# Kernel optimization log

Hardware: AMD Instinct MI355X
Metric: run time of the kernel (lower is better)

Reference implementation:

```python
import jax, jax.numpy as jnp
import numpy as np

ALPHA, GAMMA = 0.25, 2.0
IMG_FM, STRIDE = 96, 8


def _make_anchors():
    sizes = np.array([32.0, 64.0, 128.0], np.float32)
    ratios = np.array([0.5, 1.0, 2.0], np.float32)
    c = (np.arange(IMG_FM, dtype=np.float32) + 0.5) * STRIDE
    cy, cx = np.meshgrid(c, c, indexing="ij")
    hs = (sizes[:, None] * np.sqrt(ratios)[None, :]).reshape(-1)
    ws = (sizes[:, None] / np.sqrt(ratios)[None, :]).reshape(-1)
    y1 = cy[..., None] - hs / 2
    x1 = cx[..., None] - ws / 2
    y2 = cy[..., None] + hs / 2
    x2 = cx[..., None] + ws / 2
    # anchor layout (y1, x1, y2, x2), matching anchor_widths = a[:,3]-a[:,1]
    return np.stack([y1, x1, y2, x2], axis=-1).reshape(-1, 4).astype(np.float32)


def setup_inputs() -> dict:
    B, C, N = 4, 80, 32
    EMB, IDS, H, W = 128, 500, IMG_FM, IMG_FM
    A = IMG_FM * IMG_FM * 9
    key = jax.random.key(0)
    ks = jax.random.split(key, 8)
    cls = jax.random.uniform(ks[0], (B, A, C), jnp.float32)
    reg = jax.random.normal(ks[1], (B, A, 4), jnp.float32)
    emb = jax.random.normal(ks[2], (B, EMB, H, W), jnp.float32)
    # boxes (x1, y1, x2, y2); keep x1+x2 < 768 so (x1+x2)//8 < 96
    xy1 = jax.random.uniform(ks[3], (B, N, 2), jnp.float32, 0.0, 280.0)
    wh = jax.random.uniform(ks[4], (B, N, 2), jnp.float32, 16.0, 96.0)
    boxes = jnp.concatenate([xy1, jnp.minimum(xy1 + wh, 350.0)], axis=-1)
    labels = jax.random.randint(ks[5], (B, N), 0, C).astype(jnp.int64)
    reids = jax.random.randint(ks[6], (B, N), 0, IDS).astype(jnp.int64)
    W_track = jax.random.normal(ks[7], (EMB, IDS), jnp.float32) * 0.05
    b_track = jnp.zeros((IDS,), jnp.float32)
    anchors = jnp.asarray(_make_anchors())[None]  # [1, A, 4]
    return {
        "classifications": cls,
        "regressions": reg,
        "anchors": anchors,
        "embeddings": emb,
        "gt_bboxes_2d": boxes,
        "gt_labels": labels,
        "gt_reids": reids,
        "W_track": W_track,
        "b_track": b_track,
        "emb_scale": jnp.asarray(10.0, jnp.float32),
    }


def reference(classifications, regressions, anchors, embeddings, gt_bboxes_2d,
              gt_labels, gt_reids, W_track, b_track, emb_scale):
    anchor = anchors[0]                                   # [A,4] (y1,x1,y2,x2)
    aw = anchor[:, 3] - anchor[:, 1]
    ah = anchor[:, 2] - anchor[:, 0]
    acx = anchor[:, 1] + 0.5 * aw
    acy = anchor[:, 0] + 0.5 * ah
    num_classes = classifications.shape[-1]

    def per_image(cls_p, reg, emb, boxes, labels, reids):
        cls_p = jnp.clip(cls_p, 1e-4, 1.0 - 1e-4)         # [A,C]
        # ---- IoU: anchor (y1,x1,y2,x2) vs gt (x1,y1,x2,y2), verbatim calc_iou ----
        area_b = (boxes[:, 2] - boxes[:, 0]) * (boxes[:, 3] - boxes[:, 1])  # [N]
        iw = jnp.clip(jnp.minimum(anchor[:, 3:4], boxes[:, 2]) - jnp.maximum(anchor[:, 1:2], boxes[:, 0]), 0.0)
        ih = jnp.clip(jnp.minimum(anchor[:, 2:3], boxes[:, 3]) - jnp.maximum(anchor[:, 0:1], boxes[:, 1]), 0.0)
        inter = iw * ih                                   # [A,N]
        ua = jnp.clip(((anchor[:, 2] - anchor[:, 0]) * (anchor[:, 3] - anchor[:, 1]))[:, None] + area_b - inter, 1e-8)
        iou = inter / ua                                  # [A,N]
        iou_max = iou.max(axis=1)                         # [A]
        iou_arg = iou.argmax(axis=1)                      # [A]
        pos = iou_max >= 0.5
        neg = iou_max < 0.4
        num_pos = pos.sum().astype(cls_p.dtype)
        # ---- focal classification loss ----
        assigned_lab = labels[iou_arg]                    # [A]
        onehot = jax.nn.one_hot(assigned_lab, num_classes, dtype=cls_p.dtype)
        targets = jnp.where(pos[:, None], onehot,
                            jnp.where(neg[:, None], 0.0, -1.0))
        is_one = targets == 1.0
        af = jnp.where(is_one, ALPHA, 1.0 - ALPHA)
        fw = af * jnp.where(is_one, 1.0 - cls_p, cls_p) ** GAMMA
        bce = -(targets * jnp.log(cls_p) + (1.0 - targets) * jnp.log(1.0 - cls_p))
        cls_loss = jnp.where(targets != -1.0, fw * bce, 0.0).sum() / jnp.maximum(num_pos, 1.0)
        ab = boxes[iou_arg]                               # [A,4]
        gw = ab[:, 2] - ab[:, 0]
        gh = ab[:, 3] - ab[:, 1]
        gcx = ab[:, 0] + 0.5 * gw
        gcy = ab[:, 1] + 0.5 * gh
        gw = jnp.clip(gw, 1.0)
        gh = jnp.clip(gh, 1.0)
        tdy = (gcy - acy) / ah
        tdx = (gcx - acx) / aw
        tdh = jnp.log(gh / ah)
        tdw = jnp.log(gw / aw)
        tgt = jnp.stack([tdy, tdx, tdh, tdw], axis=1)     # [A,4]
        d = jnp.abs(tgt - reg)
        rl = jnp.where(d <= 1.0 / 9.0, 0.5 * 9.0 * d * d, d - 0.5 / 9.0)
        reg_loss = (rl * pos[:, None]).sum() / jnp.maximum(num_pos * 4.0, 1.0)
        # ---- ReID tracking loss ----
        c, h, w = emb.shape
        cx_i = jnp.floor((boxes[:, 0] + boxes[:, 2]) / 8.0)  # faithful (x1+x2)//8
        cy_i = jnp.floor((boxes[:, 1] + boxes[:, 3]) / 8.0)
        ind = (cy_i * w + cx_i).astype(jnp.int32)         # [N]
        feat = jnp.transpose(emb, (1, 2, 0)).reshape(h * w, c)[ind]  # [N,c]
        nrm = jnp.sqrt((feat * feat).sum(axis=1, keepdims=True))
        feat = emb_scale * feat / jnp.maximum(nrm, 1e-12)
        logits = feat @ W_track + b_track                 # [N, IDS]
        logp = jax.nn.log_softmax(logits, axis=-1)
        valid = (reids >= 0).astype(logp.dtype)
        ce = -jnp.take_along_axis(logp, jnp.clip(reids, 0).astype(jnp.int32)[:, None], axis=1)[:, 0]
        id_loss = (ce * valid).sum() / jnp.maximum(valid.sum(), 1.0)
        trk_loss = jnp.where(num_pos > 0, id_loss, 0.0)
        return cls_loss, reg_loss, trk_loss

    cls_l, reg_l, trk_l = jax.vmap(per_image)(
        classifications, regressions, embeddings, gt_bboxes_2d, gt_labels, gt_reids)
    return (jnp.mean(cls_l, keepdims=True),
            jnp.mean(reg_l, keepdims=True) * 50.0,
            jnp.mean(trk_l, keepdims=True))
```

## Files before the change

### kernel.cpp

```cpp
#include <hip/hip_runtime.h>
#include <cstdint>
#include <cstddef>

#define A_TOTAL 82944
#define NUM_C   80
#define NBOX    32
#define EMB_C   128
#define IDS     500
#define HW      9216
#define FM_W    96
#define BATCH   4
#define ABLK    256
#define NBLK    (A_TOTAL / ABLK)
#define REID_OFF 8192

typedef float floatx4 __attribute__((ext_vector_type(4)));

__device__ __forceinline__ float wave_sum(float v) {
#pragma unroll
    for (int o = 32; o > 0; o >>= 1) v += __shfl_down(v, o, 64);
    return v;
}
__device__ __forceinline__ float wave_max(float v) {
#pragma unroll
    for (int o = 32; o > 0; o >>= 1) v = fmaxf(v, __shfl_down(v, o, 64));
    return v;
}

__global__ __launch_bounds__(256) void assign_focal_reg_kernel(
    const float* __restrict__ cls, const float* __restrict__ reg,
    const float* __restrict__ anchors, const float* __restrict__ boxes,
    const int* __restrict__ labels, float* __restrict__ part)
{
    const int b   = blockIdx.y;
    const int a0  = blockIdx.x * ABLK;
    const int tid = threadIdx.x;

    __shared__ float4 sbox[NBOX];
    __shared__ int    slab[NBOX];
    __shared__ int    slabenc[ABLK];
    __shared__ float  sgate[ABLK];
    __shared__ float  sred[3][4];

    if (tid < NBOX) {
        sbox[tid] = ((const float4*)boxes)[b * NBOX + tid];
        slab[tid] = labels[b * NBOX + tid];
    }
    __syncthreads();

    const int a = a0 + tid;
    const float4 an = ((const float4*)anchors)[a];
    const float area_a = (an.z - an.x) * (an.w - an.y);
    float best = -1.f; int arg = 0;
#pragma unroll
    for (int n = 0; n < NBOX; ++n) {
        const float4 bx = sbox[n];
        float iw = fmaxf(fminf(an.w, bx.z) - fmaxf(an.y, bx.x), 0.f);
        float ih = fmaxf(fminf(an.z, bx.w) - fmaxf(an.x, bx.y), 0.f);
        float inter = iw * ih;
        float area_b = (bx.z - bx.x) * (bx.w - bx.y);
        float ua  = fmaxf(area_a + area_b - inter, 1e-8f);
        float iou = inter / ua;
        if (iou > best) { best = iou; arg = n; }
    }
    const bool pos = best >= 0.5f;
    const bool neg = best < 0.4f;
    slabenc[tid] = pos ? slab[arg] : -1;
    sgate[tid]   = (pos || neg) ? 1.f : 0.f;

    float reg_part = 0.f, np_part = 0.f;
    if (pos) {
        np_part = 1.f;
        const float4 ab = sbox[arg];
        float gw  = ab.z - ab.x, gh = ab.w - ab.y;
        float gcx = ab.x + 0.5f * gw, gcy = ab.y + 0.5f * gh;
        gw = fmaxf(gw, 1.f); gh = fmaxf(gh, 1.f);
        const float aw  = an.w - an.y, ah = an.z - an.x;
        const float acx = an.y + 0.5f * aw, acy = an.x + 0.5f * ah;
        const float t0 = (gcy - acy) / ah;
        const float t1 = (gcx - acx) / aw;
        const float t2 = logf(gh / ah);
        const float t3 = logf(gw / aw);
        const float4 rg = ((const float4*)reg)[(size_t)b * A_TOTAL + a];
        float dd[4] = { fabsf(t0 - rg.x), fabsf(t1 - rg.y),
                        fabsf(t2 - rg.z), fabsf(t3 - rg.w) };
#pragma unroll
        for (int k = 0; k < 4; ++k) {
            const float d = dd[k];
            reg_part += (d <= (1.f/9.f)) ? (4.5f * d * d) : (d - (0.5f/9.f));
        }
    }
    __syncthreads();

    const floatx4* crow =
        (const floatx4*)(cls + ((size_t)b * A_TOTAL + a0) * NUM_C);
    const float LO = 1e-4f;
    const float HI = (float)(1.0 - 1e-4);
    float cls_part = 0.f;
#pragma unroll
    for (int g = 0; g < 4; ++g) {
        floatx4 buf[5];
#pragma unroll
        for (int i = 0; i < 5; ++i) {
            const int f = tid + (g * 5 + i) * 256;
            buf[i] = __builtin_nontemporal_load(&crow[f]);
        }
#pragma unroll
        for (int i = 0; i < 5; ++i) {
            const int f    = tid + (g * 5 + i) * 256;
            const int row  = f / 20;
            const int col4 = f - row * 20;
            const int rel  = slabenc[row] - col4 * 4;
            const float gate = sgate[row];
            const float pv[4] = { buf[i].x, buf[i].y, buf[i].z, buf[i].w };
            float acc4 = 0.f;
#pragma unroll
            for (int j = 0; j < 4; ++j) {
                const float p  = fminf(fmaxf(pv[j], LO), HI);
                const bool one = (rel == j);
                const float w  = one ? (1.f - p) : p;
                const float af = one ? 0.25f : 0.75f;
                acc4 += af * w * w * (-__logf(1.f - w));
            }
            cls_part = fmaf(acc4, gate, cls_part);
        }
    }

    const float w0 = wave_sum(cls_part);
    const float w1 = wave_sum(reg_part);
    const float w2 = wave_sum(np_part);
    const int wid = tid >> 6, lane = tid & 63;
    if (lane == 0) { sred[0][wid] = w0; sred[1][wid] = w1; sred[2][wid] = w2; }
    __syncthreads();
    if (tid == 0) {
        float* o = part + ((size_t)b * NBLK + blockIdx.x) * 4;
        o[0] = sred[2][0] + sred[2][1] + sred[2][2] + sred[2][3];
        o[1] = sred[0][0] + sred[0][1] + sred[0][2] + sred[0][3];
        o[2] = sred[1][0] + sred[1][1] + sred[1][2] + sred[1][3];
    }
}

__global__ __launch_bounds__(512) void reid_kernel(
    const float* __restrict__ emb, const float* __restrict__ boxes,
    const int* __restrict__ reids, const float* __restrict__ Wt,
    const float* __restrict__ bt, const float* __restrict__ emb_scale,
    float* __restrict__ ws)
{
    const int b   = blockIdx.y;
    const int n   = blockIdx.x;
    const int tid = threadIdx.x;

    __shared__ float sfeat[EMB_C];
    __shared__ float slog[IDS];
    __shared__ float sred[8];
    __shared__ float sb[2];

    const float4 bx = ((const float4*)boxes)[b * NBOX + n];
    const int cx = (int)floorf((bx.x + bx.z) * 0.125f);
    const int cy = (int)floorf((bx.y + bx.w) * 0.125f);
    const int ind = cy * FM_W + cx;

    float sq = 0.f;
    if (tid < EMB_C) {
        const float v = emb[((size_t)b * EMB_C + tid) * HW + ind];
        sfeat[tid] = v;
        sq = v * v;
    }
    const float wsq = wave_sum(sq);
    if ((tid & 63) == 0) sred[tid >> 6] = wsq;
    __syncthreads();
    if (tid == 0) {
        const float nrm = sqrtf(sred[0] + sred[1]);
        sb[0] = emb_scale[0] / fmaxf(nrm, 1e-12f);
    }
    __syncthreads();
    if (tid < EMB_C) sfeat[tid] *= sb[0];
    __syncthreads();

    if (tid < IDS) {
        float al = bt[tid];
#pragma unroll 16
        for (int c = 0; c < EMB_C; ++c) al += sfeat[c] * Wt[c * IDS + tid];
        slog[tid] = al;
    }
    __syncthreads();

    float m = (tid < IDS) ? slog[tid] : -1e30f;
    m = wave_max(m);
    if ((tid & 63) == 0) sred[tid >> 6] = m;
    __syncthreads();
    if (tid == 0) {
        float mm = sred[0];
#pragma unroll
        for (int i = 1; i < 8; ++i) mm = fmaxf(mm, sred[i]);
        sb[1] = mm;
    }
    __syncthreads();
    m = sb[1];

    float se = (tid < IDS) ? expf(slog[tid] - m) : 0.f;
    se = wave_sum(se);
    if ((tid & 63) == 0) sred[tid >> 6] = se;
    __syncthreads();
    if (tid == 0) {
        float sum = 0.f;
#pragma unroll
        for (int i = 0; i < 8; ++i) sum += sred[i];
        const int rid = reids[b * NBOX + n];
        const float valid = (rid >= 0) ? 1.f : 0.f;
        const int t = rid < 0 ? 0 : rid;
        const float ce = -(slog[t] - m - logf(sum));
        float* o = ws + REID_OFF + ((size_t)b * NBOX + n) * 2;
        o[0] = ce * valid;
        o[1] = valid;
    }
}

__global__ __launch_bounds__(256) void finalize_kernel(
    const float* __restrict__ ws, float* __restrict__ out)
{
    __shared__ float s[BATCH][3];
    const int tid  = threadIdx.x;
    const int b    = tid >> 6;
    const int lane = tid & 63;

    float np = 0.f, cl = 0.f, rg = 0.f, ce = 0.f, va = 0.f;
    for (int i = lane; i < NBLK; i += 64) {
        const float* p = ws + ((size_t)b * NBLK + i) * 4;
        np += p[0]; cl += p[1]; rg += p[2];
    }
    if (lane < NBOX) {
        const float* r = ws + REID_OFF + ((size_t)b * NBOX + lane) * 2;
        ce = r[0]; va = r[1];
    }
    np = wave_sum(np); cl = wave_sum(cl); rg = wave_sum(rg);
    ce = wave_sum(ce); va = wave_sum(va);
    if (lane == 0) {
        const float cls_l = cl / fmaxf(np, 1.f);
        const float reg_l = rg / fmaxf(np * 4.f, 1.f);
        const float id_l  = ce / fmaxf(va, 1.f);
        s[b][0] = cls_l;
        s[b][1] = reg_l;
        s[b][2] = (np > 0.f) ? id_l : 0.f;
    }
    __syncthreads();
    if (tid == 0) {
        out[0] = (s[0][0] + s[1][0] + s[2][0] + s[3][0]) * 0.25f;
        out[1] = (s[0][1] + s[1][1] + s[2][1] + s[3][1]) * 0.25f * 50.f;
        out[2] = (s[0][2] + s[1][2] + s[2][2] + s[3][2]) * 0.25f;
    }
}

extern "C" void kernel_launch(void* const* d_in, const int* in_sizes, int n_in,
                              void* d_out, int out_size, void* d_ws, size_t ws_size,
                              hipStream_t stream) {
    const float* cls      = (const float*)d_in[0];
    const float* reg      = (const float*)d_in[1];
    const float* anchors  = (const float*)d_in[2];
    const float* emb      = (const float*)d_in[3];
    const float* boxes    = (const float*)d_in[4];
    const int*   labels   = (const int*)d_in[5];
    const int*   reids    = (const int*)d_in[6];
    const float* Wt       = (const float*)d_in[7];
    const float* bt       = (const float*)d_in[8];
    const float* escale   = (const float*)d_in[9];
    float* out = (float*)d_out;
    float* ws  = (float*)d_ws;

    dim3 g1(NBLK, BATCH);
    assign_focal_reg_kernel<<<g1, dim3(256), 0, stream>>>(cls, reg, anchors,
                                                          boxes, labels, ws);
    dim3 g2(NBOX, BATCH);
    reid_kernel<<<g2, dim3(512), 0, stream>>>(emb, boxes, reids, Wt, bt,
                                              escale, ws);
    finalize_kernel<<<1, 256, 0, stream>>>(ws, out);
}
```

Before: 195.4 us.

## Fuse reid into main kernel, cull IoU via union bbox, simplify focal math

```diff
diff --git a/kernel.cpp b/kernel.cpp
--- a/kernel.cpp
+++ b/kernel.cpp
@@ -27,24 +27,117 @@
     return v;
 }
 
-__global__ __launch_bounds__(256) void assign_focal_reg_kernel(
+__global__ __launch_bounds__(256) void main_kernel(
     const float* __restrict__ cls, const float* __restrict__ reg,
     const float* __restrict__ anchors, const float* __restrict__ boxes,
-    const int* __restrict__ labels, float* __restrict__ part)
+    const int* __restrict__ labels, const float* __restrict__ emb,
+    const int* __restrict__ reids, const float* __restrict__ Wt,
+    const float* __restrict__ bt, const float* __restrict__ emb_scale,
+    float* __restrict__ ws)
 {
     const int b   = blockIdx.y;
-    const int a0  = blockIdx.x * ABLK;
     const int tid = threadIdx.x;
 
     __shared__ float4 sbox[NBOX];
     __shared__ int    slab[NBOX];
+    __shared__ float  sarea[NBOX];
+    __shared__ float4 subb;
     __shared__ int    slabenc[ABLK];
     __shared__ float  sgate[ABLK];
-    __shared__ float  sred[3][4];
-
+    __shared__ float  sred3[3][4];
+    __shared__ float  sfeat[EMB_C];
+    __shared__ float  slog[IDS];
+    __shared__ float  sredR[4];
+    __shared__ float  sb[2];
+
+    if (blockIdx.x >= NBLK) {
+        const int n = blockIdx.x - NBLK;
+        const float4 bx = ((const float4*)boxes)[b * NBOX + n];
+        const int cx = (int)floorf((bx.x + bx.z) * 0.125f);
+        const int cy = (int)floorf((bx.y + bx.w) * 0.125f);
+        const int ind = cy * FM_W + cx;
+
+        float sq = 0.f;
+        if (tid < EMB_C) {
+            const float v = emb[((size_t)b * EMB_C + tid) * HW + ind];
+            sfeat[tid] = v;
+            sq = v * v;
+        }
+        const float wsq = wave_sum(sq);
+        if ((tid & 63) == 0) sredR[tid >> 6] = wsq;
+        __syncthreads();
+        if (tid == 0) {
+            const float nrm = sqrtf(sredR[0] + sredR[1]);
+            sb[0] = emb_scale[0] / fmaxf(nrm, 1e-12f);
+        }
+        __syncthreads();
+        if (tid < EMB_C) sfeat[tid] *= sb[0];
+        __syncthreads();
+
+        const int  j1   = tid + 256;
+        const bool has1 = (j1 < IDS);
+        const float* w0col = Wt + tid;
+        const float* w1col = Wt + (has1 ? j1 : tid);
+        float al0 = bt[tid];
+        float al1 = has1 ? bt[j1] : 0.f;
+#pragma unroll 8
+        for (int c = 0; c < EMB_C; ++c) {
+            const float fv = sfeat[c];
+            al0 = fmaf(fv, w0col[c * IDS], al0);
+            al1 = fmaf(fv, w1col[c * IDS], al1);
+        }
+        slog[tid] = al0;
+        if (has1) slog[j1] = al1;
+
+        float m = has1 ? fmaxf(al0, al1) : al0;
+        m = wave_max(m);
+        if ((tid & 63) == 0) sredR[tid >> 6] = m;
+        __syncthreads();
+        if (tid == 0) {
+            float mm = sredR[0];
+#pragma unroll
+            for (int i = 1; i < 4; ++i) mm = fmaxf(mm, sredR[i]);
+            sb[1] = mm;
+        }
+        __syncthreads();
+        m = sb[1];
+
+        float se = expf(al0 - m) + (has1 ? expf(al1 - m) : 0.f);
+        se = wave_sum(se);
+        if ((tid & 63) == 0) sredR[tid >> 6] = se;
+        __syncthreads();
+        if (tid == 0) {
+            const float sum = sredR[0] + sredR[1] + sredR[2] + sredR[3];
+            const int rid = reids[b * NBOX + n];
+            const float valid = (rid >= 0) ? 1.f : 0.f;
+            const int t = rid < 0 ? 0 : rid;
+            const float ce = -(slog[t] - m - logf(sum));
+            float* o = ws + REID_OFF + ((size_t)b * NBOX + n) * 2;
+            o[0] = ce * valid;
+            o[1] = valid;
+        }
+        return;
+    }
+
+    const int a0 = blockIdx.x * ABLK;
+
+    float ux1 = 1e30f, uy1 = 1e30f, ux2 = -1e30f, uy2 = -1e30f;
     if (tid < NBOX) {
-        sbox[tid] = ((const float4*)boxes)[b * NBOX + tid];
-        slab[tid] = labels[b * NBOX + tid];
+        const float4 bx = ((const float4*)boxes)[b * NBOX + tid];
+        sbox[tid]  = bx;
+        slab[tid]  = labels[b * NBOX + tid];
+        sarea[tid] = (bx.z - bx.x) * (bx.w - bx.y);
+        ux1 = bx.x; uy1 = bx.y; ux2 = bx.z; uy2 = bx.w;
+    }
+    if (tid < 64) {
+#pragma unroll
+        for (int o = 32; o > 0; o >>= 1) {
+            ux1 = fminf(ux1, __shfl_down(ux1, o, 64));
+            uy1 = fminf(uy1, __shfl_down(uy1, o, 64));
+            ux2 = fmaxf(ux2, __shfl_down(ux2, o, 64));
+            uy2 = fmaxf(uy2, __shfl_down(uy2, o, 64));
+        }
+        if (tid == 0) subb = make_float4(ux1, uy1, ux2, uy2);
     }
     __syncthreads();
 
@@ -52,16 +145,19 @@
     const float4 an = ((const float4*)anchors)[a];
     const float area_a = (an.z - an.x) * (an.w - an.y);
     float best = -1.f; int arg = 0;
-#pragma unroll
-    for (int n = 0; n < NBOX; ++n) {
-        const float4 bx = sbox[n];
-        float iw = fmaxf(fminf(an.w, bx.z) - fmaxf(an.y, bx.x), 0.f);
-        float ih = fmaxf(fminf(an.z, bx.w) - fmaxf(an.x, bx.y), 0.f);
-        float inter = iw * ih;
-        float area_b = (bx.z - bx.x) * (bx.w - bx.y);
-        float ua  = fmaxf(area_a + area_b - inter, 1e-8f);
-        float iou = inter / ua;
-        if (iou > best) { best = iou; arg = n; }
+    const float4 ub = subb;
+    if (fminf(an.w, ub.z) > fmaxf(an.y, ub.x) &&
+        fminf(an.z, ub.w) > fmaxf(an.x, ub.y)) {
+#pragma unroll
+        for (int n = 0; n < NBOX; ++n) {
+            const float4 bx = sbox[n];
+            float iw = fmaxf(fminf(an.w, bx.z) - fmaxf(an.y, bx.x), 0.f);
+            float ih = fmaxf(fminf(an.z, bx.w) - fmaxf(an.x, bx.y), 0.f);
+            float inter = iw * ih;
+            float ua  = fmaxf(area_a + sarea[n] - inter, 1e-8f);
+            float iou = inter / ua;
+            if (iou > best) { best = iou; arg = n; }
+        }
     }
     const bool pos = best >= 0.5f;
     const bool neg = best < 0.4f;
@@ -111,18 +207,23 @@
             const int row  = f / 20;
             const int col4 = f - row * 20;
             const int rel  = slabenc[row] - col4 * 4;
-            const float gate = sgate[row];
+            const float gm = sgate[row] * -0.75f;
             const float pv[4] = { buf[i].x, buf[i].y, buf[i].z, buf[i].w };
             float acc4 = 0.f;
 #pragma unroll
             for (int j = 0; j < 4; ++j) {
-                const float p  = fminf(fmaxf(pv[j], LO), HI);
-                const bool one = (rel == j);
-                const float w  = one ? (1.f - p) : p;
-                const float af = one ? 0.25f : 0.75f;
-                acc4 += af * w * w * (-__logf(1.f - w));
+                const float p = fminf(fmaxf(pv[j], LO), HI);
+                acc4 = fmaf(p * p, __logf(1.f - p), acc4);
             }
-            cls_part = fmaf(acc4, gate, cls_part);
+            cls_part = fmaf(acc4, gm, cls_part);
+            if ((unsigned)rel < 4u) {
+                float p = (rel == 0) ? pv[0] : (rel == 1) ? pv[1]
+                        : (rel == 2) ? pv[2] : pv[3];
+                p = fminf(fmaxf(p, LO), HI);
+                const float negT = 0.75f * p * p * (-__logf(1.f - p));
+                const float posT = 0.25f * (1.f - p) * (1.f - p) * (-__logf(p));
+                cls_part += posT - negT;
+            }
         }
     }
 
@@ -130,89 +231,13 @@
     const float w1 = wave_sum(reg_part);
     const float w2 = wave_sum(np_part);
     const int wid = tid >> 6, lane = tid & 63;
-    if (lane == 0) { sred[0][wid] = w0; sred[1][wid] = w1; sred[2][wid] = w2; }
+    if (lane == 0) { sred3[0][wid] = w0; sred3[1][wid] = w1; sred3[2][wid] = w2; }
     __syncthreads();
     if (tid == 0) {
-        float* o = part + ((size_t)b * NBLK + blockIdx.x) * 4;
-        o[0] = sred[2][0] + sred[2][1] + sred[2][2] + sred[2][3];
-        o[1] = sred[0][0] + sred[0][1] + sred[0][2] + sred[0][3];
-        o[2] = sred[1][0] + sred[1][1] + sred[1][2] + sred[1][3];
-    }
-}
-
-__global__ __launch_bounds__(512) void reid_kernel(
-    const float* __restrict__ emb, const float* __restrict__ boxes,
-    const int* __restrict__ reids, const float* __restrict__ Wt,
-    const float* __restrict__ bt, const float* __restrict__ emb_scale,
-    float* __restrict__ ws)
-{
-    const int b   = blockIdx.y;
-    const int n   = blockIdx.x;
-    const int tid = threadIdx.x;
-
-    __shared__ float sfeat[EMB_C];
-    __shared__ float slog[IDS];
-    __shared__ float sred[8];
-    __shared__ float sb[2];
-
-    const float4 bx = ((const float4*)boxes)[b * NBOX + n];
-    const int cx = (int)floorf((bx.x + bx.z) * 0.125f);
-    const int cy = (int)floorf((bx.y + bx.w) * 0.125f);
-    const int ind = cy * FM_W + cx;
-
-    float sq = 0.f;
-    if (tid < EMB_C) {
-        const float v = emb[((size_t)b * EMB_C + tid) * HW + ind];
-        sfeat[tid] = v;
-        sq = v * v;
-    }
-    const float wsq = wave_sum(sq);
-    if ((tid & 63) == 0) sred[tid >> 6] = wsq;
-    __syncthreads();
-    if (tid == 0) {
-        const float nrm = sqrtf(sred[0] + sred[1]);
-        sb[0] = emb_scale[0] / fmaxf(nrm, 1e-12f);
-    }
-    __syncthreads();
-    if (tid < EMB_C) sfeat[tid] *= sb[0];
-    __syncthreads();
-
-    if (tid < IDS) {
-        float al = bt[tid];
-#pragma unroll 16
-        for (int c = 0; c < EMB_C; ++c) al += sfeat[c] * Wt[c * IDS + tid];
-        slog[tid] = al;
-    }
-    __syncthreads();
-
-    float m = (tid < IDS) ? slog[tid] : -1e30f;
-    m = wave_max(m);
-    if ((tid & 63) == 0) sred[tid >> 6] = m;
-    __syncthreads();
-    if (tid == 0) {
-        float mm = sred[0];
-#pragma unroll
-        for (int i = 1; i < 8; ++i) mm = fmaxf(mm, sred[i]);
-        sb[1] = mm;
-    }
-    __syncthreads();
-    m = sb[1];
-
-    float se = (tid < IDS) ? expf(slog[tid] - m) : 0.f;
-    se = wave_sum(se);
-    if ((tid & 63) == 0) sred[tid >> 6] = se;
-    __syncthreads();
-    if (tid == 0) {
-        float sum = 0.f;
-#pragma unroll
-        for (int i = 0; i < 8; ++i) sum += sred[i];
-        const int rid = reids[b * NBOX + n];
-        const float valid = (rid >= 0) ? 1.f : 0.f;
-        const int t = rid < 0 ? 0 : rid;
-        const float ce = -(slog[t] - m - logf(sum));
-        float* o = ws + REID_OFF + ((size_t)b * NBOX + n) * 2;
-        o[0] = ce * valid;
-        o[1] = valid;
+        float* o = ws + ((size_t)b * NBLK + blockIdx.x) * 4;
+        o[0] = sred3[2][0] + sred3[2][1] + sred3[2][2] + sred3[2][3];
+        o[1] = sred3[0][0] + sred3[0][1] + sred3[0][2] + sred3[0][3];
+        o[2] = sred3[1][0] + sred3[1][1] + sred3[1][2] + sred3[1][3];
     }
 }
 
@@ -267,11 +292,8 @@
     float* out = (float*)d_out;
     float* ws  = (float*)d_ws;
 
-    dim3 g1(NBLK, BATCH);
-    assign_focal_reg_kernel<<<g1, dim3(256), 0, stream>>>(cls, reg, anchors,
-                                                          boxes, labels, ws);
-    dim3 g2(NBOX, BATCH);
-    reid_kernel<<<g2, dim3(512), 0, stream>>>(emb, boxes, reids, Wt, bt,
-                                              escale, ws);
+    dim3 g1(NBLK + NBOX, BATCH);
+    main_kernel<<<g1, dim3(256), 0, stream>>>(cls, reg, anchors, boxes, labels,
+                                              emb, reids, Wt, bt, escale, ws);
     finalize_kernel<<<1, 256, 0, stream>>>(ws, out);
 }
```

Result: faster. 181.5 us (-7.1%).
